# Kernel optimization log

Measured on AMD Instinct MI355X. Metric: run time of the kernel, lower is better.

The kernel has to match this reference:

```python
import jax, jax.numpy as jnp
import numpy as np

TAU = 2.0
NUM_HEADS = 8
EPS = 1e-5
SG_ALPHA = 4.0  # spikingjelly sigmoid surrogate default

@jax.custom_vjp
def spike(x):
    return (x >= 0.0).astype(x.dtype)

def _spike_fwd(x):
    return spike(x), x

def _spike_bwd(x, g):
    sg = jax.nn.sigmoid(SG_ALPHA * x)
    return (g * SG_ALPHA * sg * (1.0 - sg),)

spike.defvjp(_spike_fwd, _spike_bwd)

def lif(x_seq, v_th=1.0):
    # multi-step LIF, hard reset to 0, detach_reset; scan over time dim 0
    def step(v, xt):
        v = v + (xt - v) / TAU
        s = spike(v - v_th)
        v = v * (1.0 - jax.lax.stop_gradient(s))
        return v, s
    _, s = jax.lax.scan(step, jnp.zeros_like(x_seq[0]), x_seq)
    return s

def conv1x1_bn(y, W, b, g, beta, m, var):
    # y: (T,B,C,H,W), W: (Cout,Cin) -- 1x1 conv == channel GEMM; BN in eval mode
    z = jnp.einsum('tbchw,oc->tbohw', y, W)
    if b is not None:
        z = z + b.reshape(1, 1, -1, 1, 1)
    scale = (g * jax.lax.rsqrt(var + EPS)).reshape(1, 1, -1, 1, 1)
    shift = (beta - g * m * jax.lax.rsqrt(var + EPS)).reshape(1, 1, -1, 1, 1)
    return z * scale + shift

def setup_inputs() -> dict:
    key = jax.random.key(0)
    ks = jax.random.split(key, 8)
    T, B, C, H, W = 4, 32, 512, 16, 16
    d = {"x": jax.random.normal(ks[0], (T, B, C, H, W), jnp.float32)}
    d["gate_w"] = jax.random.normal(ks[1], (C, C), jnp.float32) * 0.02
    d["gate_b"] = jnp.zeros((C,), jnp.float32)
    d["q_w"] = jax.random.normal(ks[2], (C, C), jnp.float32) * 0.02
    d["k_w"] = jax.random.normal(ks[3], (C, C), jnp.float32) * 0.02
    d["proj_w"] = jax.random.normal(ks[4], (C, C), jnp.float32) * 0.02
    d["proj_b"] = jnp.zeros((C,), jnp.float32)
    for nm, kk in (("gate", ks[5]), ("q", ks[6]), ("k", ks[7]), ("proj", ks[1])):
        d[nm + "_bn_g"] = jnp.ones((C,), jnp.float32)
        d[nm + "_bn_b"] = jnp.zeros((C,), jnp.float32)
        d[nm + "_bn_m"] = jax.random.normal(kk, (C,), jnp.float32) * 0.1
        d[nm + "_bn_v"] = jnp.ones((C,), jnp.float32)
    return d

def reference(x, gate_w, gate_b, q_w, k_w, proj_w, proj_b,
              gate_bn_g, gate_bn_b, gate_bn_m, gate_bn_v,
              q_bn_g, q_bn_b, q_bn_m, q_bn_v,
              k_bn_g, k_bn_b, k_bn_m, k_bn_v,
              proj_bn_g, proj_bn_b, proj_bn_m, proj_bn_v):
    T, B, C, H, W = x.shape
    N = H * W
    h = NUM_HEADS
    Ch = C // h
    identity = x
    xs = lif(x)  # first_lif
    gate = lif(conv1x1_bn(xs, gate_w, gate_b, gate_bn_g, gate_bn_b, gate_bn_m, gate_bn_v))
    qc = lif(conv1x1_bn(xs, q_w, None, q_bn_g, q_bn_b, q_bn_m, q_bn_v))
    kc = lif(conv1x1_bn(xs, k_w, None, k_bn_g, k_bn_b, k_bn_m, k_bn_v))
    def to_heads(y):
        # (T,B,C,H,W) -> (T,B,heads,N,Ch)
        return y.reshape(T, B, C, N).transpose(0, 1, 3, 2).reshape(T, B, N, h, Ch).transpose(0, 1, 3, 2, 4)
    q = to_heads(qc)
    k = to_heads(kc)
    v = to_heads(kc)  # source bug: x_conv_out undefined; v shares the k pathway
    kv = (k * v).sum(axis=-2, keepdims=True)  # (T,B,h,1,Ch)
    kv = lif(kv, v_th=0.5)  # talking_heads_lif
    a = q * kv  # (T,B,h,N,Ch)
    a = a.transpose(0, 1, 2, 4, 3).reshape(T, B, C, H, W)
    a = a * gate
    out = conv1x1_bn(a, proj_w, proj_b, proj_bn_g, proj_bn_b, proj_bn_m, proj_bn_v) + identity
    return (out, v)
```

## Files before the change

### kernel.cpp

```cpp
#include <hip/hip_runtime.h>
#include <math.h>


typedef __bf16 bf16x8 __attribute__((ext_vector_type(8)));
typedef float f32x4 __attribute__((ext_vector_type(4)));

#define OFF_WB    0u
#define OFF_SS    2097152u
#define OFF_XS    2113536u
#define OFF_GS    35667968u
#define OFF_QS    69222400u
#define OFF_KV    102776832u
#define OFF_KVACC 102907904u

__device__ __forceinline__ unsigned short f2bf(float f) {
  unsigned u = __float_as_uint(f);
  u += 0x7fffu + ((u >> 16) & 1u);
  return (unsigned short)(u >> 16);
}

__device__ __forceinline__ void gload16(const void* g, void* l) {
  __builtin_amdgcn_global_load_lds(
      (const __attribute__((address_space(1))) void*)g,
      (__attribute__((address_space(3))) void*)l, 16, 0, 0);
}

struct PrepParams {
  const float* W[4];
  const float* bias2[2];
  const float* g[4]; const float* be[4]; const float* m[4]; const float* v[4];
};

__global__ __launch_bounds__(256) void prep_kernel(PrepParams p, unsigned char* __restrict__ ws) {
  int w = blockIdx.x, o = blockIdx.y;
  const float* Ws = p.W[w];
  unsigned short* Wb = (unsigned short*)(ws + OFF_WB) + (size_t)w * 262144;
  for (int c = threadIdx.x; c < 512; c += 256)
    Wb[o * 512 + c] = f2bf(Ws[o * 512 + c]);
  if (threadIdx.x == 0) {
    float g = p.g[w][o], be = p.be[w][o], mm = p.m[w][o], vv = p.v[w][o];
    float rs = 1.0f / sqrtf(vv + 1e-5f);
    float scale = g * rs;
    float bias = (w == 0) ? p.bias2[0][o] : ((w == 3) ? p.bias2[1][o] : 0.0f);
    float* ss = (float*)(ws + OFF_SS) + w * 1024;
    ss[o] = scale;
    ss[512 + o] = be - g * mm * rs + scale * bias;
  }
}

__global__ __launch_bounds__(256) void lif1_kernel(const float* __restrict__ x,
                                                   unsigned char* __restrict__ ws) {
  __shared__ unsigned short sp[4][32][65];
  int tid = threadIdx.x;
  int b = blockIdx.z, c0 = blockIdx.y * 32, n0 = blockIdx.x * 64;
  int nl = tid & 63, cb = tid >> 6;
#pragma unroll
  for (int g = 0; g < 8; ++g) {
    int cl = cb + g * 4;
    size_t base = ((size_t)b * 512 + (size_t)(c0 + cl)) * 256 + n0 + nl;
    float v = 0.f;
#pragma unroll
    for (int t = 0; t < 4; ++t) {
      float xv = x[base + (size_t)t * 4194304];
      v += (xv - v) * 0.5f;
      bool s = (v >= 1.f);
      v = s ? 0.f : v;
      sp[t][cl][nl] = s ? 0x3f80 : 0;
    }
  }
  __syncthreads();
  unsigned short* xs = (unsigned short*)(ws + OFF_XS);
#pragma unroll
  for (int it = 0; it < 2; ++it) {
    int s = it * 256 + tid;
    int half = s & 1, n_l = (s >> 1) & 63, t = s >> 7;
    union { unsigned short u[16]; uint4 q[2]; } pk;
#pragma unroll
    for (int j = 0; j < 16; ++j) pk.u[j] = sp[t][half * 16 + j][n_l];
    size_t off = ((size_t)(t * 32 + b) * 256 + (size_t)(n0 + n_l)) * 512 + c0 + half * 16;
    *(uint4*)(xs + off) = pk.q[0];
    *(uint4*)(xs + off + 8) = pk.q[1];
  }
}

__global__ __launch_bounds__(256, 3) void gemm3_kernel(unsigned char* __restrict__ ws,
                                                       float* __restrict__ vout,
                                                       float* __restrict__ kvacc) {
  __shared__ __align__(16) unsigned short lA[128 * 64];
  __shared__ __align__(16) unsigned short lB[64 * 64];
  __shared__ unsigned short lT[128 * 65];
  int tid = threadIdx.x;
  int w = blockIdx.z >> 5, b = blockIdx.z & 31;
  int o0 = blockIdx.y * 128, n0 = blockIdx.x * 64;
  int lane = tid & 63, wid = tid >> 6;
  int wm = (wid >> 1) * 64, wn = (wid & 1) * 32;
  int l8 = lane >> 3, l7 = lane & 7;
  int swzk = (l7 ^ l8) << 3;
  int fr = lane & 15, fhi = lane >> 4;
  int swzf = (lane & 7) << 3;
  const unsigned short* Wb = (const unsigned short*)(ws + OFF_WB) + (size_t)w * 262144;
  const unsigned short* xs = (const unsigned short*)(ws + OFF_XS);
  const float* ss = (const float*)(ws + OFF_SS) + w * 1024;
  unsigned short* spout = (w == 0) ? (unsigned short*)(ws + OFF_GS)
                                   : (unsigned short*)(ws + OFF_QS);

  float vstate[4][2][4];
#pragma unroll
  for (int mf = 0; mf < 4; ++mf)
#pragma unroll
    for (int nf = 0; nf < 2; ++nf)
#pragma unroll
      for (int r = 0; r < 4; ++r) vstate[mf][nf][r] = 0.f;

  for (int t = 0; t < 4; ++t) {
    f32x4 acc[4][2];
#pragma unroll
    for (int mf = 0; mf < 4; ++mf)
#pragma unroll
      for (int nf = 0; nf < 2; ++nf) acc[mf][nf] = (f32x4){0.f, 0.f, 0.f, 0.f};
    const unsigned short* xrow = xs + ((size_t)(t * 32 + b) * 256 + n0) * 512;

    for (int ks = 0; ks < 8; ++ks) {
      __syncthreads();
#pragma unroll
      for (int i = 0; i < 4; ++i) {
        int r = wid * 32 + i * 8 + l8;
        gload16(Wb + (size_t)(o0 + r) * 512 + ks * 64 + swzk, lA + wid * 2048 + i * 512);
      }
#pragma unroll
      for (int i = 0; i < 2; ++i) {
        int r = wid * 16 + i * 8 + l8;
        gload16(xrow + (size_t)r * 512 + ks * 64 + swzk, lB + wid * 1024 + i * 512);
      }
      __syncthreads();
#pragma unroll
      for (int ksub = 0; ksub < 2; ++ksub) {
        int kof = (ksub * 32 + fhi * 8) ^ swzf;
        bf16x8 af[4], bfr[2];
#pragma unroll
        for (int mf = 0; mf < 4; ++mf)
          af[mf] = *(const bf16x8*)&lA[(wm + mf * 16 + fr) * 64 + kof];
#pragma unroll
        for (int nf = 0; nf < 2; ++nf)
          bfr[nf] = *(const bf16x8*)&lB[(wn + nf * 16 + fr) * 64 + kof];
#pragma unroll
        for (int mf = 0; mf < 4; ++mf)
#pragma unroll
          for (int nf = 0; nf < 2; ++nf)
            acc[mf][nf] = __builtin_amdgcn_mfma_f32_16x16x32_bf16(
                af[mf], bfr[nf], acc[mf][nf], 0, 0, 0);
      }
    }
    __syncthreads();
#pragma unroll
    for (int mf = 0; mf < 4; ++mf)
#pragma unroll
      for (int nf = 0; nf < 2; ++nf)
#pragma unroll
        for (int r = 0; r < 4; ++r) {
          int ol = wm + mf * 16 + (lane >> 4) * 4 + r;
          int nn = wn + nf * 16 + (lane & 15);
          int o = o0 + ol;
          float val = acc[mf][nf][r] * ss[o] + ss[512 + o];
          float vs = vstate[mf][nf][r];
          vs += (val - vs) * 0.5f;
          bool s = (vs >= 1.f);
          vstate[mf][nf][r] = s ? 0.f : vs;
          lT[ol * 65 + nn] = s ? 0x3f80 : 0;
        }
    __syncthreads();
    if (w < 2) {
#pragma unroll
      for (int it = 0; it < 2; ++it) {
        int s = it * 256 + tid;
        int n_l = s >> 3, oc = (s & 7) * 16;
        union { unsigned short u[16]; uint4 q[2]; } pk;
#pragma unroll
        for (int j = 0; j < 16; ++j) pk.u[j] = lT[(oc + j) * 65 + n_l];
        size_t off = ((size_t)(t * 32 + b) * 256 + (size_t)(n0 + n_l)) * 512 + o0 + oc;
        *(uint4*)(spout + off) = pk.q[0];
        *(uint4*)(spout + off + 8) = pk.q[1];
      }
    } else {
#pragma unroll
      for (int it = 0; it < 4; ++it) {
        int s = it * 256 + tid;
        int n_l = s >> 4, oc = (s & 15) * 8;
        int o = o0 + oc;
        int h = o >> 6, ch = o & 63;
        float4 f0, f1;
        f0.x = lT[(oc + 0) * 65 + n_l] ? 1.f : 0.f;
        f0.y = lT[(oc + 1) * 65 + n_l] ? 1.f : 0.f;
        f0.z = lT[(oc + 2) * 65 + n_l] ? 1.f : 0.f;
        f0.w = lT[(oc + 3) * 65 + n_l] ? 1.f : 0.f;
        f1.x = lT[(oc + 4) * 65 + n_l] ? 1.f : 0.f;
        f1.y = lT[(oc + 5) * 65 + n_l] ? 1.f : 0.f;
        f1.z = lT[(oc + 6) * 65 + n_l] ? 1.f : 0.f;
        f1.w = lT[(oc + 7) * 65 + n_l] ? 1.f : 0.f;
        size_t off = (((size_t)(t * 32 + b) * 8 + h) * 256 + (size_t)(n0 + n_l)) * 64 + ch;
        *(float4*)(vout + off) = f0;
        *(float4*)(vout + off + 4) = f1;
      }
      {
        int o = tid >> 1, nh = (tid & 1) * 32;
        int cnt = 0;
#pragma unroll
        for (int n = 0; n < 32; ++n) cnt += (lT[o * 65 + nh + n] ? 1 : 0);
        cnt += __shfl_xor(cnt, 1);
        if ((tid & 1) == 0)
          kvacc[((size_t)(t * 32 + b) * 4 + blockIdx.x) * 512 + o0 + o] = (float)cnt;
      }
    }
  }
}

__global__ __launch_bounds__(256) void kv_kernel(const float* __restrict__ kvacc,
                                                 unsigned char* __restrict__ ws) {
  int b = blockIdx.x;
  unsigned short* kvs = (unsigned short*)(ws + OFF_KV);
#pragma unroll
  for (int j = 0; j < 2; ++j) {
    int c = j * 256 + threadIdx.x;
    float vm = 0.f;
#pragma unroll
    for (int t = 0; t < 4; ++t) {
      const float* p = kvacc + (size_t)(t * 32 + b) * 2048 + c;
      float tot = p[0] + p[512] + p[1024] + p[1536];
      vm += (tot - vm) * 0.5f;
      bool s = (vm >= 0.5f);
      vm = s ? 0.f : vm;
      kvs[(size_t)(t * 32 + b) * 512 + c] = s ? 0x3f80 : 0;
    }
  }
}

__global__ __launch_bounds__(256, 3) void proj_kernel(const unsigned char* __restrict__ ws,
                                                      const float* __restrict__ x,
                                                      float* __restrict__ out) {
  __shared__ __align__(16) unsigned short lA[128 * 64];
  __shared__ __align__(16) unsigned short lB[128 * 72];
  int tid = threadIdx.x;
  int t = blockIdx.z >> 5, b = blockIdx.z & 31;
  int o0 = blockIdx.y * 128, n0 = blockIdx.x * 128;
  int lane = tid & 63, wid = tid >> 6;
  int wm = (wid >> 1) * 64, wn = (wid & 1) * 64;
  int l8 = lane >> 3, l7 = lane & 7;
  int swzk = (l7 ^ l8) << 3;
  int fr = lane & 15, fhi = lane >> 4;
  int swzf = (lane & 7) << 3;
  const unsigned short* Wb = (const unsigned short*)(ws + OFF_WB) + (size_t)3 * 262144;
  const unsigned short* qs =
      (const unsigned short*)(ws + OFF_QS) + ((size_t)(t * 32 + b) * 256 + n0) * 512;
  const unsigned short* gs =
      (const unsigned short*)(ws + OFF_GS) + ((size_t)(t * 32 + b) * 256 + n0) * 512;
  const unsigned short* kvp =
      (const unsigned short*)(ws + OFF_KV) + (size_t)(t * 32 + b) * 512;
  const float* ss = (const float*)(ws + OFF_SS) + 3 * 1024;

  f32x4 acc[4][4];
#pragma unroll
  for (int mf = 0; mf < 4; ++mf)
#pragma unroll
    for (int nf = 0; nf < 4; ++nf) acc[mf][nf] = (f32x4){0.f, 0.f, 0.f, 0.f};

  for (int ks = 0; ks < 8; ++ks) {
    __syncthreads();
#pragma unroll
    for (int i = 0; i < 4; ++i) {
      int r = wid * 32 + i * 8 + l8;
      gload16(Wb + (size_t)(o0 + r) * 512 + ks * 64 + swzk, lA + wid * 2048 + i * 512);
    }
#pragma unroll
    for (int i = 0; i < 4; ++i) {
      int s = i * 256 + tid;
      int r = s >> 3, kc = (s & 7) * 8;
      size_t e = (size_t)r * 512 + ks * 64 + kc;
      uint4 qv = *(const uint4*)(qs + e);
      uint4 gv = *(const uint4*)(gs + e);
      uint4 kvv = *(const uint4*)(kvp + ks * 64 + kc);
      uint4 av;
      av.x = qv.x & gv.x & kvv.x;
      av.y = qv.y & gv.y & kvv.y;
      av.z = qv.z & gv.z & kvv.z;
      av.w = qv.w & gv.w & kvv.w;
      *(uint4*)&lB[r * 72 + kc] = av;
    }
    __syncthreads();
#pragma unroll
    for (int ksub = 0; ksub < 2; ++ksub) {
      int kofA = (ksub * 32 + fhi * 8) ^ swzf;
      int kofB = ksub * 32 + fhi * 8;
      bf16x8 af[4], bfr[4];
#pragma unroll
      for (int mf = 0; mf < 4; ++mf)
        af[mf] = *(const bf16x8*)&lA[(wm + mf * 16 + fr) * 64 + kofA];
#pragma unroll
      for (int nf = 0; nf < 4; ++nf)
        bfr[nf] = *(const bf16x8*)&lB[(wn + nf * 16 + fr) * 72 + kofB];
#pragma unroll
      for (int mf = 0; mf < 4; ++mf)
#pragma unroll
        for (int nf = 0; nf < 4; ++nf)
          acc[mf][nf] = __builtin_amdgcn_mfma_f32_16x16x32_bf16(
              af[mf], bfr[nf], acc[mf][nf], 0, 0, 0);
    }
  }
#pragma unroll
  for (int mf = 0; mf < 4; ++mf)
#pragma unroll
    for (int r = 0; r < 4; ++r) {
      int o = o0 + wm + mf * 16 + (lane >> 4) * 4 + r;
      float scale = ss[o], shift = ss[512 + o];
#pragma unroll
      for (int nf = 0; nf < 4; ++nf) {
        int nn = n0 + wn + nf * 16 + (lane & 15);
        size_t idx = ((size_t)(t * 32 + b) * 512 + o) * 256 + nn;
        out[idx] = acc[mf][nf][r] * scale + shift + x[idx];
      }
    }
}

extern "C" void kernel_launch(void* const* d_in, const int* in_sizes, int n_in,
                              void* d_out, int out_size, void* d_ws, size_t ws_size,
                              hipStream_t stream) {
  const float* x = (const float*)d_in[0];
  unsigned char* ws = (unsigned char*)d_ws;
  float* out = (float*)d_out;
  float* vout = out + 16777216;
  float* kvacc = (float*)(ws + OFF_KVACC);

  PrepParams p;
  p.W[0] = (const float*)d_in[1];
  p.W[1] = (const float*)d_in[3];
  p.W[2] = (const float*)d_in[4];
  p.W[3] = (const float*)d_in[5];
  p.bias2[0] = (const float*)d_in[2];
  p.bias2[1] = (const float*)d_in[6];
  const int bni[4] = {7, 11, 15, 19};
  for (int w = 0; w < 4; ++w) {
    p.g[w]  = (const float*)d_in[bni[w] + 0];
    p.be[w] = (const float*)d_in[bni[w] + 1];
    p.m[w]  = (const float*)d_in[bni[w] + 2];
    p.v[w]  = (const float*)d_in[bni[w] + 3];
  }

  prep_kernel<<<dim3(4, 512), dim3(256), 0, stream>>>(p, ws);
  lif1_kernel<<<dim3(4, 16, 32), dim3(256), 0, stream>>>(x, ws);
  gemm3_kernel<<<dim3(4, 4, 96), dim3(256), 0, stream>>>(ws, vout, kvacc);
  kv_kernel<<<dim3(32), dim3(256), 0, stream>>>(kvacc, ws);
  proj_kernel<<<dim3(2, 4, 128), dim3(256), 0, stream>>>(ws, x, out);
}
```

Before: 370.0 us.

## Process two timesteps per GEMM pass to reuse weight tiles; vectorize LIF loads

The gate/q/k GEMM now computes two timesteps together, loading each weight tile into LDS once and reusing it against two activation tiles. This halves weight traffic and barrier count per timestep, at the cost of doubling accumulator and LIF-state registers, which may lower occupancy under the 3-blocks launch bound. The first LIF kernel also switches to float4 loads of x, with each thread handling four spatial positions.

```diff
diff --git a/kernel.cpp b/kernel.cpp
--- a/kernel.cpp
+++ b/kernel.cpp
@@ -53,19 +53,27 @@
   __shared__ unsigned short sp[4][32][65];
   int tid = threadIdx.x;
   int b = blockIdx.z, c0 = blockIdx.y * 32, n0 = blockIdx.x * 64;
-  int nl = tid & 63, cb = tid >> 6;
-#pragma unroll
-  for (int g = 0; g < 8; ++g) {
-    int cl = cb + g * 4;
-    size_t base = ((size_t)b * 512 + (size_t)(c0 + cl)) * 256 + n0 + nl;
-    float v = 0.f;
+  int nq = (tid & 15) * 4;
+  int cl0 = tid >> 4;
+#pragma unroll
+  for (int ch = 0; ch < 2; ++ch) {
+    int cl = ch * 16 + cl0;
+    size_t base = ((size_t)b * 512 + (size_t)(c0 + cl)) * 256 + n0 + nq;
+    float4 v = {0.f, 0.f, 0.f, 0.f};
 #pragma unroll
     for (int t = 0; t < 4; ++t) {
-      float xv = x[base + (size_t)t * 4194304];
-      v += (xv - v) * 0.5f;
-      bool s = (v >= 1.f);
-      v = s ? 0.f : v;
-      sp[t][cl][nl] = s ? 0x3f80 : 0;
+      float4 xv = *(const float4*)(x + base + (size_t)t * 4194304);
+      v.x += (xv.x - v.x) * 0.5f;
+      v.y += (xv.y - v.y) * 0.5f;
+      v.z += (xv.z - v.z) * 0.5f;
+      v.w += (xv.w - v.w) * 0.5f;
+      bool s0 = (v.x >= 1.f), s1 = (v.y >= 1.f), s2 = (v.z >= 1.f), s3 = (v.w >= 1.f);
+      v.x = s0 ? 0.f : v.x;  v.y = s1 ? 0.f : v.y;
+      v.z = s2 ? 0.f : v.z;  v.w = s3 ? 0.f : v.w;
+      sp[t][cl][nq + 0] = s0 ? 0x3f80 : 0;
+      sp[t][cl][nq + 1] = s1 ? 0x3f80 : 0;
+      sp[t][cl][nq + 2] = s2 ? 0x3f80 : 0;
+      sp[t][cl][nq + 3] = s3 ? 0x3f80 : 0;
     }
   }
   __syncthreads();
@@ -87,7 +95,7 @@
                                                        float* __restrict__ vout,
                                                        float* __restrict__ kvacc) {
   __shared__ __align__(16) unsigned short lA[128 * 64];
-  __shared__ __align__(16) unsigned short lB[64 * 64];
+  __shared__ __align__(16) unsigned short lB[2 * 64 * 64];
   __shared__ unsigned short lT[128 * 65];
   int tid = threadIdx.x;
   int w = blockIdx.z >> 5, b = blockIdx.z & 31;
@@ -104,21 +112,26 @@
   unsigned short* spout = (w == 0) ? (unsigned short*)(ws + OFF_GS)
                                    : (unsigned short*)(ws + OFF_QS);
 
-  float vstate[4][2][4];
-#pragma unroll
-  for (int mf = 0; mf < 4; ++mf)
-#pragma unroll
-    for (int nf = 0; nf < 2; ++nf)
-#pragma unroll
-      for (int r = 0; r < 4; ++r) vstate[mf][nf][r] = 0.f;
-
-  for (int t = 0; t < 4; ++t) {
-    f32x4 acc[4][2];
+  float vstate[2][4][2][4];
+#pragma unroll
+  for (int ti = 0; ti < 2; ++ti)
 #pragma unroll
     for (int mf = 0; mf < 4; ++mf)
 #pragma unroll
-      for (int nf = 0; nf < 2; ++nf) acc[mf][nf] = (f32x4){0.f, 0.f, 0.f, 0.f};
-    const unsigned short* xrow = xs + ((size_t)(t * 32 + b) * 256 + n0) * 512;
+      for (int nf = 0; nf < 2; ++nf)
+#pragma unroll
+        for (int r = 0; r < 4; ++r) vstate[ti][mf][nf][r] = 0.f;
+
+  for (int tp = 0; tp < 2; ++tp) {
+    f32x4 acc[2][4][2];
+#pragma unroll
+    for (int ti = 0; ti < 2; ++ti)
+#pragma unroll
+      for (int mf = 0; mf < 4; ++mf)
+#pragma unroll
+        for (int nf = 0; nf < 2; ++nf) acc[ti][mf][nf] = (f32x4){0.f, 0.f, 0.f, 0.f};
+    const unsigned short* xrow0 = xs + ((size_t)((tp * 2 + 0) * 32 + b) * 256 + n0) * 512;
+    const unsigned short* xrow1 = xs + ((size_t)((tp * 2 + 1) * 32 + b) * 256 + n0) * 512;
 
     for (int ks = 0; ks < 8; ++ks) {
       __syncthreads();
@@ -130,85 +143,94 @@
 #pragma unroll
       for (int i = 0; i < 2; ++i) {
         int r = wid * 16 + i * 8 + l8;
-        gload16(xrow + (size_t)r * 512 + ks * 64 + swzk, lB + wid * 1024 + i * 512);
+        gload16(xrow0 + (size_t)r * 512 + ks * 64 + swzk, lB + wid * 1024 + i * 512);
+        gload16(xrow1 + (size_t)r * 512 + ks * 64 + swzk, lB + 4096 + wid * 1024 + i * 512);
       }
       __syncthreads();
 #pragma unroll
       for (int ksub = 0; ksub < 2; ++ksub) {
         int kof = (ksub * 32 + fhi * 8) ^ swzf;
-        bf16x8 af[4], bfr[2];
+        bf16x8 af[4], bfr[2][2];
 #pragma unroll
         for (int mf = 0; mf < 4; ++mf)
           af[mf] = *(const bf16x8*)&lA[(wm + mf * 16 + fr) * 64 + kof];
 #pragma unroll
+        for (int ti = 0; ti < 2; ++ti)
+#pragma unroll
+          for (int nf = 0; nf < 2; ++nf)
+            bfr[ti][nf] = *(const bf16x8*)&lB[ti * 4096 + (wn + nf * 16 + fr) * 64 + kof];
+#pragma unroll
+        for (int ti = 0; ti < 2; ++ti)
+#pragma unroll
+          for (int mf = 0; mf < 4; ++mf)
+#pragma unroll
+            for (int nf = 0; nf < 2; ++nf)
+              acc[ti][mf][nf] = __builtin_amdgcn_mfma_f32_16x16x32_bf16(
+                  af[mf], bfr[ti][nf], acc[ti][mf][nf], 0, 0, 0);
+      }
+    }
+#pragma unroll
+    for (int ti = 0; ti < 2; ++ti) {
+      int t = tp * 2 + ti;
+      __syncthreads();
+#pragma unroll
+      for (int mf = 0; mf < 4; ++mf)
+#pragma unroll
         for (int nf = 0; nf < 2; ++nf)
-          bfr[nf] = *(const bf16x8*)&lB[(wn + nf * 16 + fr) * 64 + kof];
-#pragma unroll
-        for (int mf = 0; mf < 4; ++mf)
-#pragma unroll
-          for (int nf = 0; nf < 2; ++nf)
-            acc[mf][nf] = __builtin_amdgcn_mfma_f32_16x16x32_bf16(
-                af[mf], bfr[nf], acc[mf][nf], 0, 0, 0);
-      }
-    }
-    __syncthreads();
-#pragma unroll
-    for (int mf = 0; mf < 4; ++mf)
-#pragma unroll
-      for (int nf = 0; nf < 2; ++nf)
-#pragma unroll
-        for (int r = 0; r < 4; ++r) {
-          int ol = wm + mf * 16 + (lane >> 4) * 4 + r;
-          int nn = wn + nf * 16 + (lane & 15);
-          int o = o0 + ol;
-          float val = acc[mf][nf][r] * ss[o] + ss[512 + o];
-          float vs = vstate[mf][nf][r];
-          vs += (val - vs) * 0.5f;
-          bool s = (vs >= 1.f);
-          vstate[mf][nf][r] = s ? 0.f : vs;
-          lT[ol * 65 + nn] = s ? 0x3f80 : 0;
+#pragma unroll
+          for (int r = 0; r < 4; ++r) {
+            int ol = wm + mf * 16 + (lane >> 4) * 4 + r;
+            int nn = wn + nf * 16 + (lane & 15);
+            int o = o0 + ol;
+            float val = acc[ti][mf][nf][r] * ss[o] + ss[512 + o];
+            float vs = vstate[ti][mf][nf][r];
+            vs += (val - vs) * 0.5f;
+            bool s = (vs >= 1.f);
+            vstate[ti][mf][nf][r] = s ? 0.f : vs;
+            lT[ol * 65 + nn] = s ? 0x3f80 : 0;
+          }
+      __syncthreads();
+      if (w < 2) {
+#pragma unroll
+        for (int it = 0; it < 2; ++it) {
+          int s = it * 256 + tid;
+          int n_l = s >> 3, oc = (s & 7) * 16;
+          union { unsigned short u[16]; uint4 q[2]; } pk;
+#pragma unroll
+          for (int j = 0; j < 16; ++j) pk.u[j] = lT[(oc + j) * 65 + n_l];
+          size_t off = ((size_t)(t * 32 + b) * 256 + (size_t)(n0 + n_l)) * 512 + o0 + oc;
+          *(uint4*)(spout + off) = pk.q[0];
+          *(uint4*)(spout + off + 8) = pk.q[1];
         }
-    __syncthreads();
-    if (w < 2) {
-#pragma unroll
-      for (int it = 0; it < 2; ++it) {
-        int s = it * 256 + tid;
-        int n_l = s >> 3, oc = (s & 7) * 16;
-        union { unsigned short u[16]; uint4 q[2]; } pk;
-#pragma unroll
-        for (int j = 0; j < 16; ++j) pk.u[j] = lT[(oc + j) * 65 + n_l];
-        size_t off = ((size_t)(t * 32 + b) * 256 + (size_t)(n0 + n_l)) * 512 + o0 + oc;
-        *(uint4*)(spout + off) = pk.q[0];
-        *(uint4*)(spout + off + 8) = pk.q[1];
-      }
-    } else {
-#pragma unroll
-      for (int it = 0; it < 4; ++it) {
-        int s = it * 256 + tid;
-        int n_l = s >> 4, oc = (s & 15) * 8;
-        int o = o0 + oc;
-        int h = o >> 6, ch = o & 63;
-        float4 f0, f1;
-        f0.x = lT[(oc + 0) * 65 + n_l] ? 1.f : 0.f;
-        f0.y = lT[(oc + 1) * 65 + n_l] ? 1.f : 0.f;
-        f0.z = lT[(oc + 2) * 65 + n_l] ? 1.f : 0.f;
-        f0.w = lT[(oc + 3) * 65 + n_l] ? 1.f : 0.f;
-        f1.x = lT[(oc + 4) * 65 + n_l] ? 1.f : 0.f;
-        f1.y = lT[(oc + 5) * 65 + n_l] ? 1.f : 0.f;
-        f1.z = lT[(oc + 6) * 65 + n_l] ? 1.f : 0.f;
-        f1.w = lT[(oc + 7) * 65 + n_l] ? 1.f : 0.f;
-        size_t off = (((size_t)(t * 32 + b) * 8 + h) * 256 + (size_t)(n0 + n_l)) * 64 + ch;
-        *(float4*)(vout + off) = f0;
-        *(float4*)(vout + off + 4) = f1;
-      }
-      {
-        int o = tid >> 1, nh = (tid & 1) * 32;
-        int cnt = 0;
-#pragma unroll
-        for (int n = 0; n < 32; ++n) cnt += (lT[o * 65 + nh + n] ? 1 : 0);
-        cnt += __shfl_xor(cnt, 1);
-        if ((tid & 1) == 0)
-          kvacc[((size_t)(t * 32 + b) * 4 + blockIdx.x) * 512 + o0 + o] = (float)cnt;
+      } else {
+#pragma unroll
+        for (int it = 0; it < 4; ++it) {
+          int s = it * 256 + tid;
+          int n_l = s >> 4, oc = (s & 15) * 8;
+          int o = o0 + oc;
+          int h = o >> 6, chn = o & 63;
+          float4 f0, f1;
+          f0.x = lT[(oc + 0) * 65 + n_l] ? 1.f : 0.f;
+          f0.y = lT[(oc + 1) * 65 + n_l] ? 1.f : 0.f;
+          f0.z = lT[(oc + 2) * 65 + n_l] ? 1.f : 0.f;
+          f0.w = lT[(oc + 3) * 65 + n_l] ? 1.f : 0.f;
+          f1.x = lT[(oc + 4) * 65 + n_l] ? 1.f : 0.f;
+          f1.y = lT[(oc + 5) * 65 + n_l] ? 1.f : 0.f;
+          f1.z = lT[(oc + 6) * 65 + n_l] ? 1.f : 0.f;
+          f1.w = lT[(oc + 7) * 65 + n_l] ? 1.f : 0.f;
+          size_t off = (((size_t)(t * 32 + b) * 8 + h) * 256 + (size_t)(n0 + n_l)) * 64 + chn;
+          *(float4*)(vout + off) = f0;
+          *(float4*)(vout + off + 4) = f1;
+        }
+        {
+          int o = tid >> 1, nh = (tid & 1) * 32;
+          int cnt = 0;
+#pragma unroll
+          for (int n = 0; n < 32; ++n) cnt += (lT[o * 65 + nh + n] ? 1 : 0);
+          cnt += __shfl_xor(cnt, 1);
+          if ((tid & 1) == 0)
+            kvacc[((size_t)(t * 32 + b) * 4 + blockIdx.x) * 512 + o0 + o] = (float)cnt;
+        }
       }
     }
   }
```

New measurement: 491.5 us. 32.8% more time.
